# Performance work log

Measured on AMD Instinct MI355X. Metric: run time of the kernel, lower is better.

The kernel has to match this reference:

```python
import jax, jax.numpy as jnp
import numpy as np

ETA = 0.01   # Hebbian learning rate of the plasticity rule
LR = 1.0     # CircuitModel.lr


def setup_inputs() -> dict:
    key = jax.random.key(0)
    k1, k2, k3 = jax.random.split(key, 3)
    B, T, NI, NO, NOBS = 64, 256, 512, 512, 128
    X = jax.random.normal(k1, (B, T, NI), dtype=jnp.float32)
    W_init = jax.random.normal(k2, (B, NO, NI), dtype=jnp.float32) * 0.1
    observed_idx = jnp.sort(jax.random.randint(k3, (NOBS,), 0, NO))
    return {"X": X, "W_init": W_init, "observed_idx": observed_idx}


def reference(X, W_init, observed_idx):
    # X: [B,T,NI], W_init: [B,NO,NI], observed_idx: [NOBS] int
    NO = W_init.shape[1]
    mask = jnp.zeros((NO,), X.dtype).at[observed_idx].set(1.0)  # [NO]

    def step(W, x_t):
        # x_t: [B,NI]
        pre = jnp.einsum('boi,bi->bo', W, x_t)          # [B,NO]
        y = jax.nn.sigmoid(pre)
        m = y[:, observed_idx]                           # [B,NOBS] recorded before masking
        y_sparse = y * mask                              # zero unobserved outputs
        W = W * mask[None, :, None]                      # zero unobserved rows of W
        dW = ETA * (y_sparse[:, :, None] * x_t[:, None, :])  # Hebbian outer product
        return W + LR * dW, m

    _, m_traj = jax.lax.scan(step, W_init, jnp.swapaxes(X, 0, 1))  # [T,B,NOBS]
    return jnp.swapaxes(m_traj, 0, 1)  # [B,T,NOBS]
```

## Files before the change

kernel.cpp:

```cpp
#include <hip/hip_runtime.h>

#define NB   64
#define NT   256
#define NI   512
#define NO   512
#define NOBS 128
#define ETA  0.01f

typedef __attribute__((ext_vector_type(8))) short bf16x8;
typedef __attribute__((ext_vector_type(4))) float f32x4;

__device__ __forceinline__ unsigned short f2bf(float f) {
    unsigned int u = __float_as_uint(f);
    return (unsigned short)((u + 0x7fffu + ((u >> 16) & 1u)) >> 16);
}

__device__ __forceinline__ unsigned cvtpk(float lo, float hi) {
    unsigned r;
    asm("v_cvt_pk_bf16_f32 %0, %1, %2" : "=v"(r) : "v"(lo), "v"(hi));
    return r;
}

__global__ __launch_bounds__(256)
void k1_gemm(const float* __restrict__ Xf, const float* __restrict__ Wf,
             const int* __restrict__ obs,
             float* __restrict__ Gd, unsigned short* __restrict__ Gh,
             float* __restrict__ P0)
{
    __shared__ unsigned short As[128 * 64];
    __shared__ unsigned short Bs[128 * 64];
    __shared__ int obsS[128];

    const int tid  = threadIdx.x;
    const int lane = tid & 63;
    const int wv   = tid >> 6;
    const int l16  = lane & 15;
    const int quad = lane >> 4;

    const int bid  = blockIdx.x;
    const int xcd  = bid & 7;
    const int slot = bid >> 3;
    const int b    = xcd + 8 * (slot / 5);
    const int sub  = slot % 5;

    if (tid < 128) obsS[tid] = obs[tid];
    __syncthreads();

    int bm = 0, bn = 0;
    if (sub < 3) {
        bm = (sub >= 1) ? 1 : 0;
        bn = (sub == 2) ? 1 : 0;
    } else {
        bm = sub - 3;
    }
    const bool sameAB = (sub == 0) || (sub == 2);

    const int mrow = tid >> 3;
    const int ccol = tid & 7;
    const float* aP[4];
    const float* bP[4];
    int slotv[4];
#pragma unroll
    for (int it = 0; it < 4; ++it) {
        const int m = it * 32 + mrow;
        slotv[it] = m * 64 + ((ccol ^ (m & 7)) * 8);
        aP[it] = Xf + ((size_t)b * NT + bm * 128 + m) * NI + ccol * 8;
        bP[it] = (sub < 3)
                   ? Xf + ((size_t)b * NT + bn * 128 + m) * NI + ccol * 8
                   : Wf + ((size_t)b * NO + obsS[m]) * NI + ccol * 8;
    }

    const int wm = (wv >> 1) * 64;
    const int wn = (wv & 1) * 64;

    f32x4 acc[4][4] = {};

    for (int kb = 0; kb < NI / 64; ++kb) {
        __syncthreads();
#pragma unroll
        for (int it = 0; it < 4; ++it) {
            const float4 a0 = *(const float4*)(aP[it]);
            const float4 a1 = *(const float4*)(aP[it] + 4);
            uint4 ap;
            ap.x = cvtpk(a0.x, a0.y); ap.y = cvtpk(a0.z, a0.w);
            ap.z = cvtpk(a1.x, a1.y); ap.w = cvtpk(a1.z, a1.w);
            *(uint4*)&As[slotv[it]] = ap;
            aP[it] += 64;
            if (!sameAB) {
                const float4 b0 = *(const float4*)(bP[it]);
                const float4 b1 = *(const float4*)(bP[it] + 4);
                uint4 bp;
                bp.x = cvtpk(b0.x, b0.y); bp.y = cvtpk(b0.z, b0.w);
                bp.z = cvtpk(b1.x, b1.y); bp.w = cvtpk(b1.z, b1.w);
                *(uint4*)&Bs[slotv[it]] = bp;
            }
            bP[it] += 64;
        }
        __syncthreads();
        const unsigned short* Bsrc = sameAB ? As : Bs;
#pragma unroll
        for (int ks = 0; ks < 2; ++ks) {
            const int q = ks * 4 + quad;
            bf16x8 af[4], bfr[4];
#pragma unroll
            for (int mt = 0; mt < 4; ++mt) {
                const int m = wm + mt * 16 + l16;
                af[mt] = *(const bf16x8*)&As[m * 64 + ((q ^ (m & 7)) * 8)];
            }
#pragma unroll
            for (int nt = 0; nt < 4; ++nt) {
                const int n = wn + nt * 16 + l16;
                bfr[nt] = *(const bf16x8*)&Bsrc[n * 64 + ((q ^ (n & 7)) * 8)];
            }
#pragma unroll
            for (int mt = 0; mt < 4; ++mt)
#pragma unroll
                for (int nt = 0; nt < 4; ++nt)
                    acc[mt][nt] = __builtin_amdgcn_mfma_f32_16x16x32_bf16(
                        af[mt], bfr[nt], acc[mt][nt], 0, 0, 0);
        }
    }

    if (sub < 3) {
        unsigned short* GhB = Gh + ((size_t)b << 16);
        float* GdB = Gd + ((size_t)b << 12);
#pragma unroll
        for (int mt = 0; mt < 4; ++mt)
#pragma unroll
            for (int nt = 0; nt < 4; ++nt) {
                const int gcol = bn * 128 + wn + nt * 16 + l16;
#pragma unroll
                for (int r = 0; r < 4; ++r) {
                    const int grow = bm * 128 + wm + mt * 16 + quad * 4 + r;
                    const float v = ETA * acc[mt][nt][r];
                    GhB[(size_t)grow * 256 + gcol] = f2bf(v);
                    if ((grow >> 4) == (gcol >> 4))
                        GdB[((grow >> 4) << 8) + ((grow & 15) << 4) + (gcol & 15)] = v;
                }
            }
    } else {
        float* Pb = P0 + (size_t)b * NT * NOBS + (size_t)bm * 128 * NOBS;
#pragma unroll
        for (int mt = 0; mt < 4; ++mt)
#pragma unroll
            for (int nt = 0; nt < 4; ++nt)
#pragma unroll
                for (int r = 0; r < 4; ++r)
                    Pb[(size_t)(wm + mt * 16 + quad * 4 + r) * NOBS
                       + wn + nt * 16 + l16] = acc[mt][nt][r];
    }
}


#define LDROW(Q0, Q1, Q2, Q3, U1)                                          \
    {                                                                      \
        if ((U1) <= 14) {                                                  \
            if ((U1) <= 2)  Q0 = *(const f32x4*)(gdc + (U1) * 16);         \
            if ((U1) <= 6)  Q1 = *(const f32x4*)(gdc + (U1) * 16 + 4);     \
            if ((U1) <= 10) Q2 = *(const f32x4*)(gdc + (U1) * 16 + 8);     \
            Q3 = *(const f32x4*)(gdc + (U1) * 16 + 12);                    \
        }                                                                  \
    }

#define GV(Q0, Q1, Q2, Q3, V)                                              \
    ((V) < 4 ? (Q0)[(V) & 3] : (V) < 8 ? (Q1)[(V) & 3]                     \
             : (V) < 12 ? (Q2)[(V) & 3] : (Q3)[(V) & 3])

#define SCAN_STEP(U, C0, C1, C2, C3, N0, N1, N2, N3)                       \
    {                                                                      \
        LDROW(N0, N1, N2, N3, (U) + 2)                                     \
        const float y = __builtin_amdgcn_rcpf(1.f + __expf(-p[(U)]));      \
        ob[obOff + (size_t)((U) * NOBS)] = y;                              \
        _Pragma("unroll")                                                  \
        for (int v = (U) + 1; v < 16; ++v)                                 \
            p[v] = fmaf(y, GV(C0, C1, C2, C3, v), p[v]);                   \
        if ((U) & 1)                                                       \
            ybf2[cp * 128 + ((U) >> 1) * 16 + j] =                         \
                (unsigned)f2bf(eprev) | ((unsigned)f2bf(y) << 16);         \
        else                                                               \
            eprev = y;                                                     \
    }

__global__ __launch_bounds__(512, 4)
void k2_scan(const float* __restrict__ Gd, const unsigned short* __restrict__ Gh,
             const float* __restrict__ P0, float* __restrict__ out)
{
    __shared__ float gdiag[16 * 16 * 16];
    __shared__ float preS[16 * 17];
    __shared__ unsigned int ybf2[2 * 8 * 16];

    const int tid  = threadIdx.x;
    const int lane = tid & 63;
    const int l16  = lane & 15;
    const int quad = lane >> 4;
    const int w    = __builtin_amdgcn_readfirstlane(tid >> 6);

    const int b  = blockIdx.x & 63;
    const int jg = blockIdx.x >> 6;

    const float* Pb = P0 + (size_t)b * NT * NOBS + jg * 16;
    const unsigned short* GhB = Gh + ((size_t)b << 16);
    float* ob = out + (size_t)b * NT * NOBS + jg * 16;

    {
        const f32x4* gs = (const f32x4*)(Gd + ((size_t)b << 12));
        ((f32x4*)gdiag)[tid]       = gs[tid];
        ((f32x4*)gdiag)[512 + tid] = gs[512 + tid];
    }

    f32x4 acc[2];
#pragma unroll
    for (int s2 = 0; s2 < 2; ++s2)
#pragma unroll
        for (int r = 0; r < 4; ++r)
            acc[s2][r] = Pb[(size_t)(w * 32 + s2 * 16 + quad * 4 + r) * NOBS + l16];

    const int T0 = 2 * w, T1 = 2 * w + 1;

    union AB { bf16x8 v; unsigned int d[4]; };
    AB Acur0, Acur1, Anext0, Anext1;
#pragma unroll
    for (int p2 = 0; p2 < 4; ++p2) {
        Acur0.d[p2] = 0; Acur1.d[p2] = 0; Anext0.d[p2] = 0; Anext1.d[p2] = 0;
    }
    if (quad < 2) {
        if (T0 > 0)
            Acur0.v = *(const bf16x8*)(GhB + (size_t)(T0 * 16 + l16) * 256 + quad * 8);
        Acur1.v = *(const bf16x8*)(GhB + (size_t)(T1 * 16 + l16) * 256 + quad * 8);
    }

    auto scan_chunk = [&](const int c, const f32x4 a) {
#pragma unroll
        for (int r = 0; r < 4; ++r)
            preS[(quad * 4 + r) * 17 + l16] = a[r];
        asm volatile("s_waitcnt lgkmcnt(0)" ::: "memory");
        __builtin_amdgcn_s_setprio(1);
        if (lane < 16) {
            const int j = lane;
            const int cp = c & 1;
            const float* gdc = gdiag + (c << 8);
            const size_t obOff = (size_t)(c << 4) * NOBS + j;
            float p[16];
#pragma unroll
            for (int u = 0; u < 16; ++u) p[u] = preS[u * 17 + j];
            f32x4 Aq0, Aq1, Aq2, Aq3, Bq0, Bq1, Bq2, Bq3, Cq0, Cq1, Cq2, Cq3;
            LDROW(Aq0, Aq1, Aq2, Aq3, 0)
            LDROW(Bq0, Bq1, Bq2, Bq3, 1)
            float eprev = 0.f;
            SCAN_STEP(0,  Aq0, Aq1, Aq2, Aq3, Cq0, Cq1, Cq2, Cq3)
            SCAN_STEP(1,  Bq0, Bq1, Bq2, Bq3, Aq0, Aq1, Aq2, Aq3)
            SCAN_STEP(2,  Cq0, Cq1, Cq2, Cq3, Bq0, Bq1, Bq2, Bq3)
            SCAN_STEP(3,  Aq0, Aq1, Aq2, Aq3, Cq0, Cq1, Cq2, Cq3)
            SCAN_STEP(4,  Bq0, Bq1, Bq2, Bq3, Aq0, Aq1, Aq2, Aq3)
            SCAN_STEP(5,  Cq0, Cq1, Cq2, Cq3, Bq0, Bq1, Bq2, Bq3)
            SCAN_STEP(6,  Aq0, Aq1, Aq2, Aq3, Cq0, Cq1, Cq2, Cq3)
            SCAN_STEP(7,  Bq0, Bq1, Bq2, Bq3, Aq0, Aq1, Aq2, Aq3)
            SCAN_STEP(8,  Cq0, Cq1, Cq2, Cq3, Bq0, Bq1, Bq2, Bq3)
            SCAN_STEP(9,  Aq0, Aq1, Aq2, Aq3, Cq0, Cq1, Cq2, Cq3)
            SCAN_STEP(10, Bq0, Bq1, Bq2, Bq3, Aq0, Aq1, Aq2, Aq3)
            SCAN_STEP(11, Cq0, Cq1, Cq2, Cq3, Bq0, Bq1, Bq2, Bq3)
            SCAN_STEP(12, Aq0, Aq1, Aq2, Aq3, Cq0, Cq1, Cq2, Cq3)
            SCAN_STEP(13, Bq0, Bq1, Bq2, Bq3, Aq0, Aq1, Aq2, Aq3)
            SCAN_STEP(14, Cq0, Cq1, Cq2, Cq3, Bq0, Bq1, Bq2, Bq3)
            SCAN_STEP(15, Aq0, Aq1, Aq2, Aq3, Cq0, Cq1, Cq2, Cq3)
        }
        __builtin_amdgcn_s_setprio(0);
    };

    if (w == 0)
        scan_chunk(0, acc[0]);
    __syncthreads();

#pragma unroll 1
    for (int c = 0; c < 15; ++c) {
        if (T1 > c) {
            AB B;
#pragma unroll
            for (int p2 = 0; p2 < 4; ++p2) B.d[p2] = 0;
            if (quad < 2) {
#pragma unroll
                for (int p2 = 0; p2 < 4; ++p2)
                    B.d[p2] = ybf2[(c & 1) * 128 + (quad * 4 + p2) * 16 + l16];
            }
#pragma unroll
            for (int p2 = 0; p2 < 4; ++p2) { Anext0.d[p2] = 0; Anext1.d[p2] = 0; }
            if (quad < 2) {
                if (T0 > c + 1)
                    Anext0.v = *(const bf16x8*)(GhB + (size_t)(T0 * 16 + l16) * 256
                                                + (c + 1) * 16 + quad * 8);
                if (T1 > c + 1)
                    Anext1.v = *(const bf16x8*)(GhB + (size_t)(T1 * 16 + l16) * 256
                                                + (c + 1) * 16 + quad * 8);
            }
            if (T0 > c)
                acc[0] = __builtin_amdgcn_mfma_f32_16x16x32_bf16(
                    Acur0.v, B.v, acc[0], 0, 0, 0);
            acc[1] = __builtin_amdgcn_mfma_f32_16x16x32_bf16(
                Acur1.v, B.v, acc[1], 0, 0, 0);
            if (w == ((c + 1) >> 1)) {
                if ((c + 1) & 1) scan_chunk(c + 1, acc[1]);
                else             scan_chunk(c + 1, acc[0]);
            }
            Acur0 = Anext0;
            Acur1 = Anext1;
        }
        __syncthreads();
    }
}

extern "C" void kernel_launch(void* const* d_in, const int* in_sizes, int n_in,
                              void* d_out, int out_size, void* d_ws, size_t ws_size,
                              hipStream_t stream)
{
    const float* X   = (const float*)d_in[0];
    const float* Wi  = (const float*)d_in[1];
    const int*   obs = (const int*)d_in[2];
    float*       out = (float*)d_out;

    float*          Gd = (float*)d_ws;
    float*          P0 = (float*)((char*)d_ws + (1u << 20));
    unsigned short* Gh = (unsigned short*)((char*)d_ws + (9u << 20));

    hipLaunchKernelGGL(k1_gemm, dim3(NB * 5), dim3(256), 0, stream,
                       X, Wi, obs, Gd, Gh, P0);
    hipLaunchKernelGGL(k2_scan, dim3(NB * 8), dim3(512), 0, stream,
                       Gd, Gh, P0, out);
}
```

Measured before the change: 160.0 us.

## Collapse scan kernel to single wavefront holding all sixteen chunk accumulators

The scan kernel drops from 512 threads (8 waves each owning two time chunks, with a block barrier per chunk) to one 64-lane wave that keeps all 16 chunk accumulators in registers and applies each chunk's correction MFMAs itself. This removes the per-step __syncthreads and the double-buffered ybf2 handoff between waves, at the cost of far more registers per lane and serialising the correction MFMAs in one wave. The GEMM kernel's block-to-batch mapping is also simplified, dropping the XCD-aware interleaving.

New measurement: 159.9 us. No clear change (-0.1%).

```diff
diff --git a/kernel.cpp b/kernel.cpp
--- a/kernel.cpp
+++ b/kernel.cpp
@@ -37,11 +37,8 @@
     const int l16  = lane & 15;
     const int quad = lane >> 4;
 
-    const int bid  = blockIdx.x;
-    const int xcd  = bid & 7;
-    const int slot = bid >> 3;
-    const int b    = xcd + 8 * (slot / 5);
-    const int sub  = slot % 5;
+    const int b   = blockIdx.x & 63;
+    const int sub = blockIdx.x >> 6;
 
     if (tid < 128) obsS[tid] = obs[tid];
     __syncthreads();
@@ -175,25 +172,23 @@
         for (int v = (U) + 1; v < 16; ++v)                                 \
             p[v] = fmaf(y, GV(C0, C1, C2, C3, v), p[v]);                   \
         if ((U) & 1)                                                       \
-            ybf2[cp * 128 + ((U) >> 1) * 16 + j] =                         \
+            ybf2[((U) >> 1) * 16 + j] =                                    \
                 (unsigned)f2bf(eprev) | ((unsigned)f2bf(y) << 16);         \
         else                                                               \
             eprev = y;                                                     \
     }
 
-__global__ __launch_bounds__(512, 4)
+__global__ __launch_bounds__(64)
 void k2_scan(const float* __restrict__ Gd, const unsigned short* __restrict__ Gh,
              const float* __restrict__ P0, float* __restrict__ out)
 {
     __shared__ float gdiag[16 * 16 * 16];
     __shared__ float preS[16 * 17];
-    __shared__ unsigned int ybf2[2 * 8 * 16];
-
-    const int tid  = threadIdx.x;
-    const int lane = tid & 63;
+    __shared__ unsigned int ybf2[8 * 16];
+
+    const int lane = threadIdx.x;
     const int l16  = lane & 15;
     const int quad = lane >> 4;
-    const int w    = __builtin_amdgcn_readfirstlane(tid >> 6);
 
     const int b  = blockIdx.x & 63;
     const int jg = blockIdx.x >> 6;
@@ -204,40 +199,30 @@
 
     {
         const f32x4* gs = (const f32x4*)(Gd + ((size_t)b << 12));
-        ((f32x4*)gdiag)[tid]       = gs[tid];
-        ((f32x4*)gdiag)[512 + tid] = gs[512 + tid];
-    }
-
-    f32x4 acc[2];
-#pragma unroll
-    for (int s2 = 0; s2 < 2; ++s2)
+#pragma unroll
+        for (int i = 0; i < 16; ++i)
+            ((f32x4*)gdiag)[i * 64 + lane] = gs[i * 64 + lane];
+    }
+
+    f32x4 acc[16];
+#pragma unroll
+    for (int T = 0; T < 16; ++T)
 #pragma unroll
         for (int r = 0; r < 4; ++r)
-            acc[s2][r] = Pb[(size_t)(w * 32 + s2 * 16 + quad * 4 + r) * NOBS + l16];
-
-    const int T0 = 2 * w, T1 = 2 * w + 1;
+            acc[T][r] = Pb[(size_t)(T * 16 + quad * 4 + r) * NOBS + l16];
 
     union AB { bf16x8 v; unsigned int d[4]; };
-    AB Acur0, Acur1, Anext0, Anext1;
-#pragma unroll
-    for (int p2 = 0; p2 < 4; ++p2) {
-        Acur0.d[p2] = 0; Acur1.d[p2] = 0; Anext0.d[p2] = 0; Anext1.d[p2] = 0;
-    }
-    if (quad < 2) {
-        if (T0 > 0)
-            Acur0.v = *(const bf16x8*)(GhB + (size_t)(T0 * 16 + l16) * 256 + quad * 8);
-        Acur1.v = *(const bf16x8*)(GhB + (size_t)(T1 * 16 + l16) * 256 + quad * 8);
-    }
+    AB Af[16];
 
     auto scan_chunk = [&](const int c, const f32x4 a) {
 #pragma unroll
         for (int r = 0; r < 4; ++r)
             preS[(quad * 4 + r) * 17 + l16] = a[r];
         asm volatile("s_waitcnt lgkmcnt(0)" ::: "memory");
+        __builtin_amdgcn_sched_barrier(0);
         __builtin_amdgcn_s_setprio(1);
         if (lane < 16) {
             const int j = lane;
-            const int cp = c & 1;
             const float* gdc = gdiag + (c << 8);
             const size_t obOff = (size_t)(c << 4) * NOBS + j;
             float p[16];
@@ -267,44 +252,31 @@
         __builtin_amdgcn_s_setprio(0);
     };
 
-    if (w == 0)
-        scan_chunk(0, acc[0]);
-    __syncthreads();
-
-#pragma unroll 1
-    for (int c = 0; c < 15; ++c) {
-        if (T1 > c) {
+#pragma unroll
+    for (int c = 0; c < 16; ++c) {
+#pragma unroll
+        for (int T = c + 1; T < 16; ++T) {
+#pragma unroll
+            for (int p2 = 0; p2 < 4; ++p2) Af[T].d[p2] = 0;
+            if (quad < 2)
+                Af[T].v = *(const bf16x8*)(GhB + (size_t)(T * 16 + l16) * 256
+                                           + c * 16 + quad * 8);
+        }
+        scan_chunk(c, acc[c]);
+        if (c < 15) {
             AB B;
 #pragma unroll
             for (int p2 = 0; p2 < 4; ++p2) B.d[p2] = 0;
             if (quad < 2) {
 #pragma unroll
                 for (int p2 = 0; p2 < 4; ++p2)
-                    B.d[p2] = ybf2[(c & 1) * 128 + (quad * 4 + p2) * 16 + l16];
-            }
-#pragma unroll
-            for (int p2 = 0; p2 < 4; ++p2) { Anext0.d[p2] = 0; Anext1.d[p2] = 0; }
-            if (quad < 2) {
-                if (T0 > c + 1)
-                    Anext0.v = *(const bf16x8*)(GhB + (size_t)(T0 * 16 + l16) * 256
-                                                + (c + 1) * 16 + quad * 8);
-                if (T1 > c + 1)
-                    Anext1.v = *(const bf16x8*)(GhB + (size_t)(T1 * 16 + l16) * 256
-                                                + (c + 1) * 16 + quad * 8);
-            }
-            if (T0 > c)
-                acc[0] = __builtin_amdgcn_mfma_f32_16x16x32_bf16(
-                    Acur0.v, B.v, acc[0], 0, 0, 0);
-            acc[1] = __builtin_amdgcn_mfma_f32_16x16x32_bf16(
-                Acur1.v, B.v, acc[1], 0, 0, 0);
-            if (w == ((c + 1) >> 1)) {
-                if ((c + 1) & 1) scan_chunk(c + 1, acc[1]);
-                else             scan_chunk(c + 1, acc[0]);
-            }
-            Acur0 = Anext0;
-            Acur1 = Anext1;
-        }
-        __syncthreads();
+                    B.d[p2] = ybf2[(quad * 4 + p2) * 16 + l16];
+            }
+#pragma unroll
+            for (int T = c + 1; T < 16; ++T)
+                acc[T] = __builtin_amdgcn_mfma_f32_16x16x32_bf16(
+                    Af[T].v, B.v, acc[T], 0, 0, 0);
+        }
     }
 }
 
@@ -323,6 +295,6 @@
 
     hipLaunchKernelGGL(k1_gemm, dim3(NB * 5), dim3(256), 0, stream,
                        X, Wi, obs, Gd, Gh, P0);
-    hipLaunchKernelGGL(k2_scan, dim3(NB * 8), dim3(512), 0, stream,
+    hipLaunchKernelGGL(k2_scan, dim3(NB * 8), dim3(64), 0, stream,
                        Gd, Gh, P0, out);
 }
```
